# Performance work log

Hardware: AMD Instinct MI355X
Metric: run time of the kernel (lower is better)

Reference implementation:

```python
import jax, jax.numpy as jnp
import numpy as np

DIM = 1024
RATIO = 4
B, N = 4, 4096
EPS = 1e-5


def setup_inputs() -> dict:
    key = jax.random.key(0)
    ks = jax.random.split(key, 9)
    s = 0.02
    d, dr = DIM, DIM * RATIO
    return {
        "x": jax.random.normal(ks[0], (B, N, d), dtype=jnp.float32),
        "ln_g": jnp.ones((d,), dtype=jnp.float32),
        "ln_b": jnp.zeros((d,), dtype=jnp.float32),
        "Wq": jax.random.normal(ks[1], (d, d), dtype=jnp.float32) * s,
        "bq": jnp.zeros((d,), dtype=jnp.float32),
        "Wk": jax.random.normal(ks[2], (dr, d), dtype=jnp.float32) * s,
        "bk": jnp.zeros((d,), dtype=jnp.float32),
        "Wv": jax.random.normal(ks[3], (dr, d), dtype=jnp.float32) * s,
        "bv": jnp.zeros((d,), dtype=jnp.float32),
        "Wo": jax.random.normal(ks[4], (d, d), dtype=jnp.float32) * s,
        "bo": jnp.zeros((d,), dtype=jnp.float32),
    }


def reference(x, ln_g, ln_b, Wq, bq, Wk, bk, Wv, bv, Wo, bo):
    b, n, d = x.shape
    scale = jnp.sqrt(jnp.asarray(d, dtype=x.dtype))
    # LayerNorm over last dim
    mu = jnp.mean(x, axis=-1, keepdims=True)
    var = jnp.mean(jnp.square(x - mu), axis=-1, keepdims=True)
    xn = (x - mu) * jax.lax.rsqrt(var + EPS) * ln_g + ln_b
    # Q: (b, n, d)
    q = xn @ Wq + bq
    # fold ratio tokens together: (b, n/ratio, d*ratio)
    xr = xn.reshape(b, n // RATIO, d * RATIO)
    k = xr @ Wk + bk            # (b, m, d), m = n/ratio
    v = xr @ Wv + bv            # (b, m, d)
    scores = jnp.einsum("bnd,bmd->bnm", q, k) / scale
    attn = jax.nn.softmax(scores, axis=-1)
    out = jnp.einsum("bnm,bmd->bnd", attn, v)
    return out @ Wo + bo
```

## Files before the change

### kernel.cpp

```cpp
#include <hip/hip_runtime.h>
#include <hip/hip_bf16.h>
#include <stdint.h>

typedef __bf16 bf16x8 __attribute__((ext_vector_type(8)));
typedef float f32x4 __attribute__((ext_vector_type(4)));
typedef __hip_bfloat16 bf16;

#define D_MODEL 1024
#define BATCH 4
#define NSEQ 4096
#define NTOK (BATCH * NSEQ)
#define MTOK (BATCH * (NSEQ / 4))

__device__ __forceinline__ void async_copy16(const void* g, void* l) {
  __builtin_amdgcn_global_load_lds(
      (const __attribute__((address_space(1))) void*)g,
      (__attribute__((address_space(3))) void*)l, 16, 0, 0);
}

__device__ __forceinline__ float to_f32(float v) { return v; }
__device__ __forceinline__ float to_f32(bf16 v) { return __bfloat162float(v); }

__global__ __launch_bounds__(256) void ln_kernel(
    const float* __restrict__ x, const float* __restrict__ g,
    const float* __restrict__ b, bf16* __restrict__ xn) {
  const size_t row = blockIdx.x;
  const float4* xr = (const float4*)(x + row * D_MODEL);
  const int tid = threadIdx.x;
  float4 v = xr[tid];
  float s = v.x + v.y + v.z + v.w;
  float sq = v.x * v.x + v.y * v.y + v.z * v.z + v.w * v.w;
#pragma unroll
  for (int o = 1; o < 64; o <<= 1) {
    s += __shfl_xor(s, o);
    sq += __shfl_xor(sq, o);
  }
  __shared__ float rs[4], rq[4];
  if ((tid & 63) == 0) { rs[tid >> 6] = s; rq[tid >> 6] = sq; }
  __syncthreads();
  s = rs[0] + rs[1] + rs[2] + rs[3];
  sq = rq[0] + rq[1] + rq[2] + rq[3];
  const float mu = s * (1.f / D_MODEL);
  const float var = sq * (1.f / D_MODEL) - mu * mu;
  const float rstd = rsqrtf(var + 1e-5f);
  float4 gv = ((const float4*)g)[tid];
  float4 bv = ((const float4*)b)[tid];
  union { ushort4 u; bf16 h[4]; } pk;
  pk.h[0] = __float2bfloat16((v.x - mu) * rstd * gv.x + bv.x);
  pk.h[1] = __float2bfloat16((v.y - mu) * rstd * gv.y + bv.y);
  pk.h[2] = __float2bfloat16((v.z - mu) * rstd * gv.z + bv.z);
  pk.h[3] = __float2bfloat16((v.w - mu) * rstd * gv.w + bv.w);
  ((ushort4*)(xn + row * D_MODEL))[tid] = pk.u;
}

template <typename T>
__global__ __launch_bounds__(256) void transpose_to_bf16(
    const T* __restrict__ in, bf16* __restrict__ out, int ldin, int ldout,
    size_t inStride, size_t outStride) {
  __shared__ bf16 tile[32][33];
  const int tx = threadIdx.x;
  const int ty = threadIdx.y;
  const int c0 = blockIdx.x * 32;
  const int r0 = blockIdx.y * 32;
  const T* ip = in + (size_t)blockIdx.z * inStride;
  bf16* op = out + (size_t)blockIdx.z * outStride;
#pragma unroll
  for (int i = 0; i < 4; i++) {
    const int r = r0 + ty + i * 8;
    tile[ty + i * 8][tx] = __float2bfloat16(to_f32(ip[(size_t)r * ldin + c0 + tx]));
  }
  __syncthreads();
#pragma unroll
  for (int i = 0; i < 4; i++) {
    const int oc = c0 + ty + i * 8;
    op[(size_t)oc * ldout + r0 + tx] = tile[tx][ty + i * 8];
  }
}

__global__ __launch_bounds__(256) void pack2(const float* __restrict__ a,
                                             const float* __restrict__ b,
                                             float* __restrict__ o) {
  const int i = blockIdx.x * 256 + threadIdx.x;
  o[i] = (i < 1024) ? a[i] : b[i - 1024];
}

__global__ __launch_bounds__(256) void softmax_kernel(
    const float* __restrict__ S, bf16* __restrict__ P) {
  const size_t row = blockIdx.x;
  const float4* sp = (const float4*)(S + row * 1024);
  const int tid = threadIdx.x;
  float4 v = sp[tid];
  float mx = fmaxf(fmaxf(v.x, v.y), fmaxf(v.z, v.w));
#pragma unroll
  for (int o = 1; o < 64; o <<= 1) mx = fmaxf(mx, __shfl_xor(mx, o));
  __shared__ float red[4];
  __shared__ float red2[4];
  if ((tid & 63) == 0) red[tid >> 6] = mx;
  __syncthreads();
  mx = fmaxf(fmaxf(red[0], red[1]), fmaxf(red[2], red[3]));
  const float e0 = __expf(v.x - mx), e1 = __expf(v.y - mx);
  const float e2 = __expf(v.z - mx), e3 = __expf(v.w - mx);
  float s = e0 + e1 + e2 + e3;
#pragma unroll
  for (int o = 1; o < 64; o <<= 1) s += __shfl_xor(s, o);
  if ((tid & 63) == 0) red2[tid >> 6] = s;
  __syncthreads();
  s = red2[0] + red2[1] + red2[2] + red2[3];
  const float inv = 1.f / s;
  union { ushort4 u; bf16 h[4]; } pk;
  pk.h[0] = __float2bfloat16(e0 * inv);
  pk.h[1] = __float2bfloat16(e1 * inv);
  pk.h[2] = __float2bfloat16(e2 * inv);
  pk.h[3] = __float2bfloat16(e3 * inv);
  ((ushort4*)(P + row * 1024))[tid] = pk.u;
}

template <typename CT, bool HAS_BIAS, int MFR>
__global__ __launch_bounds__(512, 1) void gemm8p(
    const bf16* __restrict__ A, const bf16* __restrict__ Bt,
    CT* __restrict__ C, const float* __restrict__ bias, float scale,
    int K, int lda, int ldb, int ldc,
    size_t aStride, size_t bStride, size_t cStride) {
  constexpr int BM = MFR * 32;
  constexpr int AHALF = MFR * 2048;
  constexpr int ABUF = MFR * 4096;
  constexpr int BUFS = ABUF + 32768;
  constexpr int AL = MFR / 4;
  __shared__ __align__(128) char lds[2 * BUFS];

  const int tid = threadIdx.x;
  const int lane = tid & 63;
  const int wid = tid >> 6;
  const int wr = wid >> 2;
  const int wc = wid & 3;

  const int nx = gridDim.x, ny = gridDim.y;
  const int shx = __popc(nx - 1), shy = __popc(ny - 1);
  const int lxy = nx * ny;
  int lin = blockIdx.x + nx * blockIdx.y + lxy * blockIdx.z;
  const int nwg = lxy * gridDim.z;
  lin = (lin & 7) * (nwg >> 3) + (lin >> 3);
  const int bx = lin & (nx - 1);
  const int by = (lin >> shx) & (ny - 1);
  const int bz = lin >> (shx + shy);

  const int bn0 = bx * 256;
  const int bm0 = by * BM;
  A += (size_t)bz * aStride;
  Bt += (size_t)bz * bStride;
  C += (size_t)bz * cStride;

  const bf16* pa[AL];
  int loA[AL];
  const bf16* pb[2];
  int loB[2];
#pragma unroll
  for (int j = 0; j < AL; j++) {
    const int o = tid * 16 + j * 8192;
    const int L = o ^ (((o >> 7) & 7) << 4);
    pa[j] = A + (size_t)(bm0 + (L >> 7)) * lda + ((L & 127) >> 1);
    loA[j] = o;
  }
#pragma unroll
  for (int j = 0; j < 2; j++) {
    const int o = tid * 16 + j * 8192;
    const int L = o ^ (((o >> 7) & 7) << 4);
    pb[j] = Bt + (size_t)(bn0 + (L >> 7)) * ldb + ((L & 127) >> 1);
    loB[j] = o;
  }

  const int arow = wr * (MFR * 16) + (lane & 15);
  const int brow = wc * 64 + (lane & 15);
  const int aLin = arow * 128 + (lane >> 4) * 16;
  const int bLin = brow * 128 + (lane >> 4) * 16;
  const int aSw = (arow & 7) << 4;
  const int bSw = (brow & 7) << 4;
  const int aRd0 = aLin ^ aSw, aRd1 = (aLin + 64) ^ aSw;
  const int bRd0 = bLin ^ bSw, bRd1 = (bLin + 64) ^ bSw;

  bf16x8 Ah[MFR / 2][2];
  bf16x8 B0f[2][2], B1f[2][2];
  f32x4 acc[MFR][4];
#pragma unroll
  for (int m = 0; m < MFR; m++)
#pragma unroll
    for (int n = 0; n < 4; n++) acc[m][n] = (f32x4){0.f, 0.f, 0.f, 0.f};

#define STAGE_A(b, h, kt) { const size_t go = (size_t)((h) * (BM / 2)) * lda + (size_t)(kt) * 64; \
  _Pragma("unroll") for (int j = 0; j < AL; j++) \
    async_copy16(pa[j] + go, lds + (b) * BUFS + (h) * AHALF + loA[j]); }
#define STAGE_B(b, h, kt) { const size_t go = (size_t)((h) * 128) * ldb + (size_t)(kt) * 64; \
  _Pragma("unroll") for (int j = 0; j < 2; j++) \
    async_copy16(pb[j] + go, lds + (b) * BUFS + ABUF + (h) * 16384 + loB[j]); }
#define READ_A(b, h) _Pragma("unroll") for (int m2 = 0; m2 < MFR / 2; m2++) \
  _Pragma("unroll") for (int kk = 0; kk < 2; kk++) \
    Ah[m2][kk] = *(const bf16x8*)(lds + (b) * BUFS + ((kk ? aRd1 : aRd0) + ((h) * (MFR / 2) + m2) * 2048));
#define READ_B0(b) _Pragma("unroll") for (int n2 = 0; n2 < 2; n2++) \
  _Pragma("unroll") for (int kk = 0; kk < 2; kk++) \
    B0f[n2][kk] = *(const bf16x8*)(lds + (b) * BUFS + ABUF + ((kk ? bRd1 : bRd0) + n2 * 2048));
#define READ_B1(b) _Pragma("unroll") for (int n2 = 0; n2 < 2; n2++) \
  _Pragma("unroll") for (int kk = 0; kk < 2; kk++) \
    B1f[n2][kk] = *(const bf16x8*)(lds + (b) * BUFS + ABUF + ((kk ? bRd1 : bRd0) + (2 + n2) * 2048));
#define MFMA_Q(MH, NH, BF) { __builtin_amdgcn_s_setprio(1); \
  _Pragma("unroll") for (int m2 = 0; m2 < MFR / 2; m2++) \
  _Pragma("unroll") for (int n2 = 0; n2 < 2; n2++) \
  _Pragma("unroll") for (int kk = 0; kk < 2; kk++) \
    acc[(MH) * (MFR / 2) + m2][(NH) * 2 + n2] = __builtin_amdgcn_mfma_f32_16x16x32_bf16( \
        Ah[m2][kk], BF[n2][kk], acc[(MH) * (MFR / 2) + m2][(NH) * 2 + n2], 0, 0, 0); \
  __builtin_amdgcn_s_setprio(0); }
#define BARR() { __builtin_amdgcn_sched_barrier(0); __builtin_amdgcn_s_barrier(); __builtin_amdgcn_sched_barrier(0); }
#define VMC4() { asm volatile("s_waitcnt vmcnt(4)" ::: "memory"); __builtin_amdgcn_sched_barrier(0); }
#define VMCN() { if constexpr (AL == 2) { asm volatile("s_waitcnt vmcnt(6)" ::: "memory"); } \
                 else { asm volatile("s_waitcnt vmcnt(4)" ::: "memory"); } \
                 __builtin_amdgcn_sched_barrier(0); }
#define VMC0() { asm volatile("s_waitcnt vmcnt(0)" ::: "memory"); __builtin_amdgcn_sched_barrier(0); }

  STAGE_A(0, 0, 0) STAGE_A(0, 1, 0) STAGE_B(0, 0, 0) STAGE_B(0, 1, 0)
  STAGE_A(1, 0, 1) STAGE_A(1, 1, 1) STAGE_B(1, 0, 1)
  VMCN()
  BARR()

  const int NIT = K >> 7;
  for (int it = 0; it < NIT - 1; ++it) {
    const int kt = it * 2;
    READ_A(0, 0) READ_B0(0)
    STAGE_B(1, 1, kt + 1)
    BARR()
    MFMA_Q(0, 0, B0f)
    BARR()
    READ_B1(0)
    BARR()
    MFMA_Q(0, 1, B1f)
    BARR()
    READ_A(0, 1)
    STAGE_B(0, 0, kt + 2)
    BARR()
    MFMA_Q(1, 0, B0f)
    BARR()
    STAGE_B(0, 1, kt + 2)
    VMC4()
    BARR()
    MFMA_Q(1, 1, B1f)
    BARR()
    READ_A(1, 0) READ_B0(1)
    STAGE_A(0, 0, kt + 2)
    BARR()
    MFMA_Q(0, 0, B0f)
    BARR()
    READ_B1(1)
    STAGE_A(0, 1, kt + 2)
    BARR()
    MFMA_Q(0, 1, B1f)
    BARR()
    READ_A(1, 1)
    STAGE_B(1, 0, kt + 3)
    BARR()
    MFMA_Q(1, 0, B0f)
    BARR()
    STAGE_A(1, 0, kt + 3) STAGE_A(1, 1, kt + 3)
    VMCN()
    BARR()
    MFMA_Q(1, 1, B1f)
    BARR()
  }
  {
    READ_A(0, 0) READ_B0(0)
    STAGE_B(1, 1, 2 * NIT - 1)
    BARR()
    MFMA_Q(0, 0, B0f)
    BARR()
    READ_B1(0)
    BARR()
    MFMA_Q(0, 1, B1f)
    BARR()
    READ_A(0, 1)
    BARR()
    MFMA_Q(1, 0, B0f)
    BARR()
    VMC0()
    BARR()
    MFMA_Q(1, 1, B1f)
    BARR()
    READ_A(1, 0) READ_B0(1)
    MFMA_Q(0, 0, B0f)
    READ_B1(1)
    MFMA_Q(0, 1, B1f)
    READ_A(1, 1)
    MFMA_Q(1, 0, B0f)
    MFMA_Q(1, 1, B1f)
  }
#undef STAGE_A
#undef STAGE_B
#undef READ_A
#undef READ_B0
#undef READ_B1
#undef MFMA_Q
#undef BARR
#undef VMC4
#undef VMCN
#undef VMC0

  const int cl = lane & 15;
  const int rg = lane >> 4;
#pragma unroll
  for (int m = 0; m < MFR; m++) {
#pragma unroll
    for (int n = 0; n < 4; n++) {
      const int col = bn0 + wc * 64 + n * 16 + cl;
      const float bv = HAS_BIAS ? bias[col] : 0.f;
#pragma unroll
      for (int j = 0; j < 4; j++) {
        const int row = bm0 + wr * (MFR * 16) + m * 16 + rg * 4 + j;
        const float v = acc[m][n][j] * scale + bv;
        if constexpr (sizeof(CT) == 2)
          C[(size_t)row * ldc + col] = __float2bfloat16(v);
        else
          C[(size_t)row * ldc + col] = v;
      }
    }
  }
}

extern "C" void kernel_launch(void* const* d_in, const int* in_sizes, int n_in,
                              void* d_out, int out_size, void* d_ws, size_t ws_size,
                              hipStream_t stream) {
  const float* x = (const float*)d_in[0];
  const float* ln_g = (const float*)d_in[1];
  const float* ln_b = (const float*)d_in[2];
  const float* Wq = (const float*)d_in[3];
  const float* bq = (const float*)d_in[4];
  const float* Wk = (const float*)d_in[5];
  const float* bk = (const float*)d_in[6];
  const float* Wv = (const float*)d_in[7];
  const float* bv = (const float*)d_in[8];
  const float* Wo = (const float*)d_in[9];
  const float* bo = (const float*)d_in[10];
  float* out = (float*)d_out;

  char* w = (char*)d_ws;
  auto alloc = [&](size_t bytes) {
    char* p = w;
    w += (bytes + 255) & ~(size_t)255;
    return p;
  };
  bf16* xn    = (bf16*)alloc((size_t)NTOK * D_MODEL * 2);
  bf16* WqT   = (bf16*)alloc((size_t)D_MODEL * D_MODEL * 2);
  bf16* WkvT  = (bf16*)alloc((size_t)2 * D_MODEL * 4 * D_MODEL * 2);
  bf16* WoT   = (bf16*)alloc((size_t)D_MODEL * D_MODEL * 2);
  float* bkv  = (float*)alloc((size_t)2048 * 4);
  bf16* q     = (bf16*)alloc((size_t)NTOK * D_MODEL * 2);
  bf16* kv    = (bf16*)alloc((size_t)MTOK * 2048 * 2);
  bf16* vT    = (bf16*)alloc((size_t)MTOK * D_MODEL * 2);
  float* sc   = (float*)alloc((size_t)NTOK * 1024 * 4);
  bf16* attn  = (bf16*)alloc((size_t)NTOK * 1024 * 2);
  bf16* aout  = q;

  ln_kernel<<<NTOK, 256, 0, stream>>>(x, ln_g, ln_b, xn);

  transpose_to_bf16<float><<<dim3(32, 32, 1), dim3(32, 8), 0, stream>>>(Wq, WqT, 1024, 1024, 0, 0);
  transpose_to_bf16<float><<<dim3(32, 128, 1), dim3(32, 8), 0, stream>>>(Wk, WkvT, 1024, 4096, 0, 0);
  transpose_to_bf16<float><<<dim3(32, 128, 1), dim3(32, 8), 0, stream>>>(
      Wv, WkvT + (size_t)1024 * 4096, 1024, 4096, 0, 0);
  transpose_to_bf16<float><<<dim3(32, 32, 1), dim3(32, 8), 0, stream>>>(Wo, WoT, 1024, 1024, 0, 0);
  pack2<<<8, 256, 0, stream>>>(bk, bv, bkv);

  gemm8p<bf16, true, 8><<<dim3(4, 64, 1), 512, 0, stream>>>(
      xn, WqT, q, bq, 1.f, 1024, 1024, 1024, 1024, 0, 0, 0);

  gemm8p<bf16, true, 4><<<dim3(8, 32, 1), 512, 0, stream>>>(
      xn, WkvT, kv, bkv, 1.f, 4096, 4096, 4096, 2048, 0, 0, 0);

  transpose_to_bf16<bf16><<<dim3(32, 32, BATCH), dim3(32, 8), 0, stream>>>(
      kv + 1024, vT, 2048, 1024, (size_t)1024 * 2048, (size_t)1024 * 1024);

  gemm8p<float, false, 8><<<dim3(4, 16, 4), 512, 0, stream>>>(
      q, kv, sc, nullptr, 0.03125f, 1024, 1024, 2048, 1024,
      (size_t)4096 * 1024, (size_t)1024 * 2048, (size_t)4096 * 1024);

  softmax_kernel<<<NTOK, 256, 0, stream>>>(sc, attn);

  gemm8p<bf16, false, 8><<<dim3(4, 16, 4), 512, 0, stream>>>(
      attn, vT, aout, nullptr, 1.f, 1024, 1024, 1024, 1024,
      (size_t)4096 * 1024, (size_t)1024 * 1024, (size_t)4096 * 1024);

  gemm8p<float, true, 8><<<dim3(4, 64, 1), 512, 0, stream>>>(
      aout, WoT, out, bo, 1.f, 1024, 1024, 1024, 1024, 0, 0, 0);
}
```

Measured before the change: 401.8 us.

## Load full A fragments per buffer and halve GEMM barrier phases

Reworks the GEMM main loop so each wave reads all A fragments of a k-buffer at once and runs two MFMA half-phases per buffer instead of four quarter-phases. This removes about half of the workgroup barriers and LDS re-read phases. The async copy staging and vmcnt waits are reordered to match. In exchange, A fragment registers double, which may lower occupancy, and the new wait counts could create hazards if they are miscounted.

New measurement: 424.1 us. +5.5%, slower.

```diff
diff --git a/kernel.cpp b/kernel.cpp
--- a/kernel.cpp
+++ b/kernel.cpp
@@ -178,7 +178,7 @@
   const int aRd0 = aLin ^ aSw, aRd1 = (aLin + 64) ^ aSw;
   const int bRd0 = bLin ^ bSw, bRd1 = (bLin + 64) ^ bSw;
 
-  bf16x8 Ah[MFR / 2][2];
+  bf16x8 Ah[MFR][2];
   bf16x8 B0f[2][2], B1f[2][2];
   f32x4 acc[MFR][4];
 #pragma unroll
@@ -192,112 +192,90 @@
 #define STAGE_B(b, h, kt) { const size_t go = (size_t)((h) * 128) * ldb + (size_t)(kt) * 64; \
   _Pragma("unroll") for (int j = 0; j < 2; j++) \
     async_copy16(pb[j] + go, lds + (b) * BUFS + ABUF + (h) * 16384 + loB[j]); }
-#define READ_A(b, h) _Pragma("unroll") for (int m2 = 0; m2 < MFR / 2; m2++) \
+#define READ_A_ALL(b) _Pragma("unroll") for (int m = 0; m < MFR; m++) \
   _Pragma("unroll") for (int kk = 0; kk < 2; kk++) \
-    Ah[m2][kk] = *(const bf16x8*)(lds + (b) * BUFS + ((kk ? aRd1 : aRd0) + ((h) * (MFR / 2) + m2) * 2048));
+    Ah[m][kk] = *(const bf16x8*)(lds + (b) * BUFS + ((kk ? aRd1 : aRd0) + m * 2048));
 #define READ_B0(b) _Pragma("unroll") for (int n2 = 0; n2 < 2; n2++) \
   _Pragma("unroll") for (int kk = 0; kk < 2; kk++) \
     B0f[n2][kk] = *(const bf16x8*)(lds + (b) * BUFS + ABUF + ((kk ? bRd1 : bRd0) + n2 * 2048));
 #define READ_B1(b) _Pragma("unroll") for (int n2 = 0; n2 < 2; n2++) \
   _Pragma("unroll") for (int kk = 0; kk < 2; kk++) \
     B1f[n2][kk] = *(const bf16x8*)(lds + (b) * BUFS + ABUF + ((kk ? bRd1 : bRd0) + (2 + n2) * 2048));
-#define MFMA_Q(MH, NH, BF) { __builtin_amdgcn_s_setprio(1); \
-  _Pragma("unroll") for (int m2 = 0; m2 < MFR / 2; m2++) \
+#define MFMA_H(NH, BF) { __builtin_amdgcn_s_setprio(1); \
+  _Pragma("unroll") for (int m = 0; m < MFR; m++) \
   _Pragma("unroll") for (int n2 = 0; n2 < 2; n2++) \
   _Pragma("unroll") for (int kk = 0; kk < 2; kk++) \
-    acc[(MH) * (MFR / 2) + m2][(NH) * 2 + n2] = __builtin_amdgcn_mfma_f32_16x16x32_bf16( \
-        Ah[m2][kk], BF[n2][kk], acc[(MH) * (MFR / 2) + m2][(NH) * 2 + n2], 0, 0, 0); \
+    acc[m][(NH) * 2 + n2] = __builtin_amdgcn_mfma_f32_16x16x32_bf16( \
+        Ah[m][kk], BF[n2][kk], acc[m][(NH) * 2 + n2], 0, 0, 0); \
   __builtin_amdgcn_s_setprio(0); }
 #define BARR() { __builtin_amdgcn_sched_barrier(0); __builtin_amdgcn_s_barrier(); __builtin_amdgcn_sched_barrier(0); }
-#define VMC4() { asm volatile("s_waitcnt vmcnt(4)" ::: "memory"); __builtin_amdgcn_sched_barrier(0); }
-#define VMCN() { if constexpr (AL == 2) { asm volatile("s_waitcnt vmcnt(6)" ::: "memory"); } \
-                 else { asm volatile("s_waitcnt vmcnt(4)" ::: "memory"); } \
-                 __builtin_amdgcn_sched_barrier(0); }
+#define VMC_A() { if constexpr (AL == 2) { asm volatile("s_waitcnt vmcnt(6)" ::: "memory"); } \
+                  else { asm volatile("s_waitcnt vmcnt(4)" ::: "memory"); } \
+                  __builtin_amdgcn_sched_barrier(0); }
+#define VMC_B() { if constexpr (AL == 2) { asm volatile("s_waitcnt vmcnt(4)" ::: "memory"); } \
+                  else { asm volatile("s_waitcnt vmcnt(2)" ::: "memory"); } \
+                  __builtin_amdgcn_sched_barrier(0); }
 #define VMC0() { asm volatile("s_waitcnt vmcnt(0)" ::: "memory"); __builtin_amdgcn_sched_barrier(0); }
 
   STAGE_A(0, 0, 0) STAGE_A(0, 1, 0) STAGE_B(0, 0, 0) STAGE_B(0, 1, 0)
   STAGE_A(1, 0, 1) STAGE_A(1, 1, 1) STAGE_B(1, 0, 1)
-  VMCN()
+  VMC_A()
   BARR()
 
   const int NIT = K >> 7;
   for (int it = 0; it < NIT - 1; ++it) {
     const int kt = it * 2;
-    READ_A(0, 0) READ_B0(0)
+    VMC_A()
+    READ_A_ALL(0) READ_B0(0)
     STAGE_B(1, 1, kt + 1)
     BARR()
-    MFMA_Q(0, 0, B0f)
+    MFMA_H(0, B0f)
     BARR()
     READ_B1(0)
-    BARR()
-    MFMA_Q(0, 1, B1f)
-    BARR()
-    READ_A(0, 1)
-    STAGE_B(0, 0, kt + 2)
-    BARR()
-    MFMA_Q(1, 0, B0f)
-    BARR()
-    STAGE_B(0, 1, kt + 2)
-    VMC4()
-    BARR()
-    MFMA_Q(1, 1, B1f)
-    BARR()
-    READ_A(1, 0) READ_B0(1)
-    STAGE_A(0, 0, kt + 2)
-    BARR()
-    MFMA_Q(0, 0, B0f)
+    STAGE_A(0, 0, kt + 2) STAGE_A(0, 1, kt + 2)
+    VMC_B()
+    BARR()
+    MFMA_H(1, B1f)
+    BARR()
+    READ_A_ALL(1) READ_B0(1)
+    STAGE_B(0, 0, kt + 2) STAGE_B(0, 1, kt + 2)
+    BARR()
+    MFMA_H(0, B0f)
     BARR()
     READ_B1(1)
-    STAGE_A(0, 1, kt + 2)
-    BARR()
-    MFMA_Q(0, 1, B1f)
-    BARR()
-    READ_A(1, 1)
-    STAGE_B(1, 0, kt + 3)
-    BARR()
-    MFMA_Q(1, 0, B0f)
-    BARR()
-    STAGE_A(1, 0, kt + 3) STAGE_A(1, 1, kt + 3)
-    VMCN()
-    BARR()
-    MFMA_Q(1, 1, B1f)
+    STAGE_A(1, 0, kt + 3) STAGE_A(1, 1, kt + 3) STAGE_B(1, 0, kt + 3)
+    BARR()
+    MFMA_H(1, B1f)
     BARR()
   }
   {
-    READ_A(0, 0) READ_B0(0)
+    VMC_A()
+    READ_A_ALL(0) READ_B0(0)
     STAGE_B(1, 1, 2 * NIT - 1)
     BARR()
-    MFMA_Q(0, 0, B0f)
+    MFMA_H(0, B0f)
     BARR()
     READ_B1(0)
-    BARR()
-    MFMA_Q(0, 1, B1f)
-    BARR()
-    READ_A(0, 1)
-    BARR()
-    MFMA_Q(1, 0, B0f)
-    BARR()
     VMC0()
     BARR()
-    MFMA_Q(1, 1, B1f)
-    BARR()
-    READ_A(1, 0) READ_B0(1)
-    MFMA_Q(0, 0, B0f)
+    MFMA_H(1, B1f)
+    BARR()
+    READ_A_ALL(1) READ_B0(1)
+    BARR()
+    MFMA_H(0, B0f)
+    BARR()
     READ_B1(1)
-    MFMA_Q(0, 1, B1f)
-    READ_A(1, 1)
-    MFMA_Q(1, 0, B0f)
-    MFMA_Q(1, 1, B1f)
+    MFMA_H(1, B1f)
   }
 #undef STAGE_A
 #undef STAGE_B
-#undef READ_A
+#undef READ_A_ALL
 #undef READ_B0
 #undef READ_B1
-#undef MFMA_Q
+#undef MFMA_H
 #undef BARR
-#undef VMC4
-#undef VMCN
+#undef VMC_A
+#undef VMC_B
 #undef VMC0
 
   const int cl = lane & 15;
```
